# Kernel tuning notes

Hardware: AMD Instinct MI355X
Metric: run time of the kernel (lower is better)

The kernel has to match this reference:

```python
import jax, jax.numpy as jnp
import numpy as np
import math

B, C, H, W = 8, 512, 32, 32
ENC = 1024
L2 = 64
NH = 8
GROUPS = 32
EPS = 1e-5

def group_norm(x, gamma, beta):
    # x: (B, C, L) GroupNorm with 32 groups (float32)
    b, c, l = x.shape
    xg = x.reshape(b, GROUPS, (c // GROUPS) * l)
    mean = xg.mean(-1, keepdims=True)
    var = xg.var(-1, keepdims=True)
    xn = ((xg - mean) * jax.lax.rsqrt(var + EPS)).reshape(b, c, l)
    return xn * gamma[None, :, None] + beta[None, :, None]

def conv1x1(w, bias, x):
    # conv_nd(1, in, out, 1): w (out, in), x (B, in, L) -> (B, out, L)
    return jnp.einsum('oc,bcl->bol', w, x) + bias[None, :, None]

def setup_inputs() -> dict:
    key = jax.random.key(0)
    ks = jax.random.split(key, 16)
    s = lambda fan_in: 1.0 / math.sqrt(fan_in)
    inp = {
        'x': jax.random.normal(ks[0], (B, C, H, W), jnp.float32),
        'xf_out': jax.random.normal(ks[1], (B, ENC, L2), jnp.float32),
        'obj_class_embedding': jax.random.normal(ks[2], (B, ENC, L2), jnp.float32),
        'obj_bbox_embedding': jax.random.normal(ks[3], (B, ENC, L2), jnp.float32),
        'image_patch_bbox_embedding': jax.random.normal(ks[4], (B, ENC, H * W), jnp.float32),
        'key_padding_mask': jax.random.bernoulli(ks[5], 0.3, (B, L2)),
        'qkv_w': jax.random.normal(ks[6], (3 * C, C), jnp.float32) * s(C),
        'qkv_b': jnp.zeros((3 * C,), jnp.float32),
        'g_qkv': jnp.ones((C,), jnp.float32),
        'b_qkv': jnp.zeros((C,), jnp.float32),
        'lc_w': jax.random.normal(ks[7], (2 * C, ENC), jnp.float32) * s(ENC),
        'lc_b': jnp.zeros((2 * C,), jnp.float32),
        'lp_w': jax.random.normal(ks[8], (C, ENC), jnp.float32) * s(ENC),
        'lp_b': jnp.zeros((C,), jnp.float32),
        'g_obj': jnp.ones((ENC,), jnp.float32),
        'b_obj': jnp.zeros((ENC,), jnp.float32),
        'g_lpos': jnp.ones((C,), jnp.float32),
        'b_lpos': jnp.zeros((C,), jnp.float32),
        'g_ipos': jnp.ones((C,), jnp.float32),
        'b_ipos': jnp.zeros((C,), jnp.float32),
        # proj_out is zero-initialized in the original (zero_module); use random
        # weights so the projection math is exercised non-trivially.
        'proj_w': jax.random.normal(ks[9], (C, C), jnp.float32) * s(C),
        'proj_b': jnp.zeros((C,), jnp.float32),
    }
    return inp

def reference(x, xf_out, obj_class_embedding, obj_bbox_embedding,
              image_patch_bbox_embedding, key_padding_mask,
              qkv_w, qkv_b, g_qkv, b_qkv, lc_w, lc_b, lp_w, lp_b,
              g_obj, b_obj, g_lpos, b_lpos, g_ipos, b_ipos, proj_w, proj_b):
    b, c, h, w = x.shape
    L1 = h * w
    d = C // NH
    xf = x.reshape(b, c, L1)

    qkv = conv1x1(qkv_w, qkv_b, group_norm(xf, g_qkv, b_qkv))  # (B, 3C, L1)
    q, k, v = jnp.split(qkv, 3, axis=1)
    q = q.reshape(b * NH, d, L1)
    k = k.reshape(b * NH, d, L1)
    v = v.reshape(b * NH, d, L1)

    ipp = group_norm(conv1x1(lp_w, lp_b, image_patch_bbox_embedding), g_ipos, b_ipos)
    ipp = ipp.reshape(b * NH, d, L1)

    q_img = jnp.concatenate([q, ipp], axis=1)  # (B*H, 2d, L1)
    k_img = jnp.concatenate([k, ipp], axis=1)

    lpe = group_norm(conv1x1(lp_w, lp_b, obj_bbox_embedding), g_lpos, b_lpos)
    lpe = lpe.reshape(b * NH, d, L2)

    lce = (xf_out + group_norm(obj_class_embedding, g_obj, b_obj)) / 2
    kl, vl = jnp.split(conv1x1(lc_w, lc_b, lce), 2, axis=1)
    kl = kl.reshape(b * NH, d, L2)
    vl = vl.reshape(b * NH, d, L2)
    k_layout = jnp.concatenate([kl, lpe], axis=1)  # (B*H, 2d, L2)

    k_mix = jnp.concatenate([k_img, k_layout], axis=2)  # (B*H, 2d, L1+L2)
    v_mix = jnp.concatenate([v, vl], axis=2)             # (B*H, d, L1+L2)

    mask = jnp.concatenate([jnp.zeros((b, L1), bool), key_padding_mask], axis=1)  # (B, L1+L2)

    scale = 1.0 / math.sqrt(math.sqrt(2 * C // NH))
    attn = jnp.einsum('bct,bcs->bts', q_img * scale, k_mix * scale)  # (B*H, L1, L1+L2)
    attn = attn.reshape(b, NH, L1, L1 + L2)
    attn = jnp.where(mask[:, None, None, :], -jnp.inf, attn)
    attn = jax.nn.softmax(attn.astype(jnp.float32), axis=-1).astype(attn.dtype)
    attn = attn.reshape(b * NH, L1, L1 + L2)

    out = jnp.einsum('bts,bcs->bct', attn, v_mix).reshape(b, C, L1)
    hproj = conv1x1(proj_w, proj_b, out)
    return (xf + hproj).reshape(b, c, h, w)
```

## Files before the change

kernel.cpp:

```cpp
#include <hip/hip_runtime.h>
#include <math.h>

#define NB 8
#define NC 512
#define NL1 1024
#define NL2 64
#define NLKV 1088
#define NENC 1024
#define EPSV 1e-5f
#define SCALE2 0.08838834764831845f
#define SCALE2Q 0.12752425f
#define DEFER_THR 11.5415603f

typedef _Float16 half8 __attribute__((ext_vector_type(8)));
typedef _Float16 half4 __attribute__((ext_vector_type(4)));
typedef __fp16 fp16x2 __attribute__((ext_vector_type(2)));
typedef float f32x4 __attribute__((ext_vector_type(4)));
typedef float f32x16 __attribute__((ext_vector_type(16)));

__device__ __forceinline__ void gload16(const _Float16* g, _Float16* l) {
  __builtin_amdgcn_global_load_lds(
      (const __attribute__((address_space(1))) void*)g,
      (__attribute__((address_space(3))) void*)l, 16, 0, 0);
}

__device__ __forceinline__ unsigned int pkrtz(float a, float b) {
  union { fp16x2 hh; unsigned int uu; } cv;
  cv.hh = __builtin_amdgcn_cvt_pkrtz(a, b);
  return cv.uu;
}

__device__ __forceinline__ float fast_exp2(float x) {
  return __builtin_amdgcn_exp2f(x);
}

__global__ __launch_bounds__(256) void k_init(
    const float* __restrict__ x, const float* __restrict__ obj,
    float* __restrict__ xm, float* __restrict__ xr,
    float* __restrict__ om, float* __restrict__ orr,
    const float* __restrict__ qkv_w, _Float16* __restrict__ w16qkv,
    const float* __restrict__ lp_w, _Float16* __restrict__ w16lp,
    const float* __restrict__ proj_w, _Float16* __restrict__ w16proj,
    const float* __restrict__ lc_w, _Float16* __restrict__ w16lc)
{
  int bid = blockIdx.x;
  if (bid < 512) {
    const float* p; float* meanp; float* rstdp; int n, bg;
    if (bid < 256) {
      bg = bid;
      int b = bg >> 5, g = bg & 31;
      p = x + ((size_t)b * 512 + (size_t)g * 16) * 1024;
      n = 16 * 1024; meanp = xm; rstdp = xr;
    } else {
      bg = bid - 256;
      int b = bg >> 5, g = bg & 31;
      p = obj + ((size_t)b * 1024 + (size_t)g * 32) * 64;
      n = 32 * 64; meanp = om; rstdp = orr;
    }
    float s = 0.f, s2 = 0.f;
    for (int i = threadIdx.x; i < n; i += 256) { float v = p[i]; s += v; s2 += v * v; }
    #pragma unroll
    for (int o = 32; o > 0; o >>= 1) { s += __shfl_down(s, o); s2 += __shfl_down(s2, o); }
    __shared__ float rs[4], rq[4];
    int lane = threadIdx.x & 63, w = threadIdx.x >> 6;
    if (lane == 0) { rs[w] = s; rq[w] = s2; }
    __syncthreads();
    if (threadIdx.x == 0) {
      float S = rs[0] + rs[1] + rs[2] + rs[3];
      float Q = rq[0] + rq[1] + rq[2] + rq[3];
      float m = S / n;
      float v = Q / n - m * m;
      if (v < 0.f) v = 0.f;
      meanp[bg] = m;
      rstdp[bg] = rsqrtf(v + EPSV);
    }
  } else {
    int cb = bid - 512;
    const float* s; _Float16* d; int i4;
    if (cb < 768)        { s = qkv_w;  d = w16qkv;  i4 = cb * 256 + threadIdx.x; }
    else if (cb < 1280)  { s = lp_w;   d = w16lp;   i4 = (cb - 768) * 256 + threadIdx.x; }
    else if (cb < 1536)  { s = proj_w; d = w16proj; i4 = (cb - 1280) * 256 + threadIdx.x; }
    else                 { s = lc_w;   d = w16lc;   i4 = (cb - 1536) * 256 + threadIdx.x; }
    float4 v = *(const float4*)&s[(size_t)i4 * 4];
    half4 o; o.x = (_Float16)v.x; o.y = (_Float16)v.y; o.z = (_Float16)v.z; o.w = (_Float16)v.w;
    *(half4*)&d[(size_t)i4 * 4] = o;
  }
}

__global__ __launch_bounds__(256) void k_prep(
    const float* __restrict__ x, const float* __restrict__ xm, const float* __restrict__ xr,
    const float* __restrict__ g_qkv, const float* __restrict__ b_qkv, _Float16* __restrict__ xT,
    const float* __restrict__ ipbe, _Float16* __restrict__ ipbeT,
    const float* __restrict__ xf_out, const float* __restrict__ obj_class,
    const float* __restrict__ obj_bbox,
    const float* __restrict__ om, const float* __restrict__ orr,
    const float* __restrict__ g_obj, const float* __restrict__ b_obj,
    _Float16* __restrict__ lceT, _Float16* __restrict__ objT)
{
  __shared__ _Float16 tile[64][72];
  const int bid = blockIdx.x;
  const int tl = threadIdx.x & 63;
  if (bid < 1024) {
    const int tt = bid & 15, ct = (bid >> 4) & 7, b = bid >> 7;
    const int c0 = ct * 64, t0 = tt * 64;
    const int cp = threadIdx.x >> 6;
    #pragma unroll
    for (int i = 0; i < 16; i++) {
      int c = c0 + i * 4 + cp;
      float v = x[((size_t)b * NC + c) * NL1 + t0 + tl];
      int g = c >> 4;
      float ga = g_qkv[c] * xr[b * 32 + g];
      float be = b_qkv[c] - xm[b * 32 + g] * ga;
      tile[tl][i * 4 + cp] = (_Float16)(v * ga + be);
    }
    __syncthreads();
    int tr = threadIdx.x >> 2, c16 = (threadIdx.x & 3) * 16;
    _Float16* dst = xT + ((size_t)b * 1024 + t0 + tr) * 512 + c0 + c16;
    *(half8*)dst = *(half8*)&tile[tr][c16];
    *(half8*)(dst + 8) = *(half8*)&tile[tr][c16 + 8];
  } else if (bid < 3072) {
    const int e2 = bid - 1024;
    const int tt = e2 & 15, et = (e2 >> 4) & 15, b = e2 >> 8;
    const int e0 = et * 64, t0 = tt * 64;
    const int ep = threadIdx.x >> 6;
    #pragma unroll
    for (int i = 0; i < 16; i++) {
      int e = e0 + i * 4 + ep;
      tile[tl][i * 4 + ep] = (_Float16)ipbe[((size_t)b * 1024 + e) * 1024 + t0 + tl];
    }
    __syncthreads();
    int tr = threadIdx.x >> 2, c16 = (threadIdx.x & 3) * 16;
    _Float16* d = ipbeT + ((size_t)b * 1024 + t0 + tr) * 1024 + e0 + c16;
    *(half8*)d = *(half8*)&tile[tr][c16];
    *(half8*)(d + 8) = *(half8*)&tile[tr][c16 + 8];
  } else {
    const int e2 = bid - 3072;
    const int et = e2 & 15, which = (e2 >> 4) & 1, b = e2 >> 5;
    const int e0 = et * 64;
    const int ep = threadIdx.x >> 6;
    if (which == 0) {
      #pragma unroll
      for (int i = 0; i < 16; i++) {
        int e = e0 + i * 4 + ep;
        size_t idx = ((size_t)b * 1024 + e) * 64 + tl;
        int g = e >> 5;
        float xn = (obj_class[idx] - om[b * 32 + g]) * orr[b * 32 + g] * g_obj[e] + b_obj[e];
        tile[tl][i * 4 + ep] = (_Float16)(0.5f * (xf_out[idx] + xn));
      }
    } else {
      #pragma unroll
      for (int i = 0; i < 16; i++) {
        int e = e0 + i * 4 + ep;
        tile[tl][i * 4 + ep] = (_Float16)obj_bbox[((size_t)b * 1024 + e) * 64 + tl];
      }
    }
    __syncthreads();
    int tr = threadIdx.x >> 2, c16 = (threadIdx.x & 3) * 16;
    _Float16* dst = (which == 0 ? lceT : objT) + ((size_t)b * 64 + tr) * 1024 + e0 + c16;
    *(half8*)dst = *(half8*)&tile[tr][c16];
    *(half8*)(dst + 8) = *(half8*)&tile[tr][c16 + 8];
  }
}

#define MFMA_CORE(KTOT)                                                                  \
  f32x4 acc[4][4];                                                                       \
  _Pragma("unroll") for (int i_ = 0; i_ < 4; i_++)                                       \
      _Pragma("unroll") for (int j_ = 0; j_ < 4; j_++) acc[i_][j_] = (f32x4)0.f;         \
  {                                                                                      \
    const int rsub = lane >> 3, csrc = (lane & 7) ^ rsub;                                \
    for (int kt = 0; kt < (KTOT); kt += 64) {                                            \
      _Pragma("unroll") for (int i = 0; i < 4; i++) {                                    \
        int seg = w * 4 + i;                                                             \
        int row = seg * 8 + rsub;                                                        \
        gload16(Abase + (size_t)(m0 + row) * (KTOT) + kt + csrc * 8, ldsA + seg * 512);  \
        gload16(Bbase + (size_t)(n0 + row) * (KTOT) + kt + csrc * 8, ldsB + seg * 512);  \
      }                                                                                  \
      __syncthreads();                                                                   \
      _Pragma("unroll") for (int kk = 0; kk < 2; kk++) {                                 \
        half8 af[4], bf[4];                                                              \
        _Pragma("unroll") for (int mb = 0; mb < 4; mb++) {                               \
          int row = wm + mb * 16 + l15;                                                  \
          af[mb] = *(const half8*)((const char*)ldsA + row * 128 +                       \
                                   ((kk * 64 + lg * 16) ^ ((row & 7) << 4)));            \
        }                                                                                \
        _Pragma("unroll") for (int nb = 0; nb < 4; nb++) {                               \
          int row = wn + nb * 16 + l15;                                                  \
          bf[nb] = *(const half8*)((const char*)ldsB + row * 128 +                       \
                                   ((kk * 64 + lg * 16) ^ ((row & 7) << 4)));            \
        }                                                                                \
        _Pragma("unroll") for (int mb = 0; mb < 4; mb++)                                 \
            _Pragma("unroll") for (int nb = 0; nb < 4; nb++)                             \
                acc[mb][nb] = __builtin_amdgcn_mfma_f32_16x16x32_f16(af[mb], bf[nb],     \
                                                                    acc[mb][nb], 0, 0, 0);\
      }                                                                                  \
      __syncthreads();                                                                   \
    }                                                                                    \
  }

#define MFMA_CORE_N64(KTOT)                                                              \
  f32x4 acc[4][2];                                                                       \
  _Pragma("unroll") for (int i_ = 0; i_ < 4; i_++)                                       \
      _Pragma("unroll") for (int j_ = 0; j_ < 2; j_++) acc[i_][j_] = (f32x4)0.f;         \
  {                                                                                      \
    const int rsub = lane >> 3, csrc = (lane & 7) ^ rsub;                                \
    for (int kt = 0; kt < (KTOT); kt += 64) {                                            \
      _Pragma("unroll") for (int i = 0; i < 4; i++) {                                    \
        int seg = w * 4 + i;                                                             \
        int row = seg * 8 + rsub;                                                        \
        gload16(Abase + (size_t)(m0 + row) * (KTOT) + kt + csrc * 8, ldsA + seg * 512);  \
      }                                                                                  \
      _Pragma("unroll") for (int i = 0; i < 2; i++) {                                    \
        int seg = w * 2 + i;                                                             \
        int row = seg * 8 + rsub;                                                        \
        gload16(Bbase + (size_t)row * (KTOT) + kt + csrc * 8, ldsB + seg * 512);         \
      }                                                                                  \
      __syncthreads();                                                                   \
      _Pragma("unroll") for (int kk = 0; kk < 2; kk++) {                                 \
        half8 af[4], bf[2];                                                              \
        _Pragma("unroll") for (int mb = 0; mb < 4; mb++) {                               \
          int row = wm + mb * 16 + l15;                                                  \
          af[mb] = *(const half8*)((const char*)ldsA + row * 128 +                       \
                                   ((kk * 64 + lg * 16) ^ ((row & 7) << 4)));            \
        }                                                                                \
        _Pragma("unroll") for (int nb = 0; nb < 2; nb++) {                               \
          int row = wn + nb * 16 + l15;                                                  \
          bf[nb] = *(const half8*)((const char*)ldsB + row * 128 +                       \
                                   ((kk * 64 + lg * 16) ^ ((row & 7) << 4)));            \
        }                                                                                \
        _Pragma("unroll") for (int mb = 0; mb < 4; mb++)                                 \
            _Pragma("unroll") for (int nb = 0; nb < 2; nb++)                             \
                acc[mb][nb] = __builtin_amdgcn_mfma_f32_16x16x32_f16(af[mb], bf[nb],     \
                                                                    acc[mb][nb], 0, 0, 0);\
      }                                                                                  \
      __syncthreads();                                                                   \
    }                                                                                    \
  }

__global__ __launch_bounds__(256) void k_mfma_big(
    const _Float16* __restrict__ w16qkv, const float* __restrict__ qkv_b,
    const _Float16* __restrict__ xhatT,
    const _Float16* __restrict__ w16lp, const float* __restrict__ lp_b,
    const _Float16* __restrict__ ipbeT,
    const _Float16* __restrict__ w16lc, const float* __restrict__ lc_b,
    const _Float16* __restrict__ lceT, const _Float16* __restrict__ objT,
    const float* __restrict__ g_lpos, const float* __restrict__ b_lpos,
    _Float16* __restrict__ qT, _Float16* __restrict__ kT, _Float16* __restrict__ vT,
    _Float16* __restrict__ ipp16)
{
  __shared__ _Float16 smem[16384];
  const int bid = blockIdx.x;
  const int tid = threadIdx.x, lane = tid & 63, w = tid >> 6;
  const int l15 = lane & 15, lg = lane >> 4;

  if (bid < 768) {
    const int nt = bid & 7, tt = bid >> 3;
    const int mt = tt % 12, b = tt / 12;
    const int m0 = mt * 128, n0 = nt * 128;
    _Float16* ldsA = smem;
    _Float16* ldsB = smem + 8192;
    const _Float16* Abase = w16qkv;
    const _Float16* Bbase = xhatT + (size_t)b * 1024 * 512;
    const int wm = (w >> 1) * 64, wn = (w & 1) * 64;
    MFMA_CORE(512)

    char* tb = (char*)smem;
    if (m0 < 1024) {
      const bool isq = (m0 < 512);
      const float qs = isq ? SCALE2Q : 1.f;
      #pragma unroll
      for (int mb = 0; mb < 4; mb++) {
        #pragma unroll
        for (int r = 0; r < 4; r++) {
          int mcol = wm + mb * 16 + lg * 4 + r;
          float bia = qkv_b[m0 + mcol];
          #pragma unroll
          for (int nb = 0; nb < 4; nb++) {
            int trow = wn + nb * 16 + l15;
            float val = (acc[mb][nb][r] + bia) * qs;
            *(_Float16*)(tb + ((trow * 256 + mcol * 2) ^ ((trow & 7) << 4))) = (_Float16)val;
          }
        }
      }
      __syncthreads();
      #pragma unroll
      for (int it = 0; it < 8; it++) {
        int e = it * 256 + tid;
        int trow = e >> 4, seg = e & 15;
        half8 v = *(const half8*)(tb + ((trow * 256 + seg * 16) ^ ((trow & 7) << 4)));
        if (isq) {
          int mq = m0 + seg * 8, hh = mq >> 6, dc = mq & 63;
          *(half8*)(qT + (((size_t)b * 8 + hh) * 1024 + n0 + trow) * 128 + dc) = v;
        } else {
          int mk = m0 - 512 + seg * 8, hh = mk >> 6, dc = mk & 63;
          *(half8*)(kT + (((size_t)b * 8 + hh) * 1088 + n0 + trow) * 128 + dc) = v;
        }
      }
    } else {
      #pragma unroll
      for (int mb = 0; mb < 4; mb++) {
        #pragma unroll
        for (int r = 0; r < 4; r++) {
          int mrow = wm + mb * 16 + lg * 4 + r;
          float bia = qkv_b[m0 + mrow];
          #pragma unroll
          for (int nb = 0; nb < 4; nb++) {
            int tcol = wn + nb * 16 + l15;
            *(_Float16*)(tb + ((mrow * 256 + tcol * 2) ^ ((mrow & 7) << 4))) =
                (_Float16)(acc[mb][nb][r] + bia);
          }
        }
      }
      __syncthreads();
      #pragma unroll
      for (int it = 0; it < 8; it++) {
        int e = it * 256 + tid;
        int mrow = e >> 4, seg = e & 15;
        half8 v = *(const half8*)(tb + ((mrow * 256 + seg * 16) ^ ((mrow & 7) << 4)));
        int mv = m0 - 1024 + mrow, hh = mv >> 6, dc = mv & 63;
        *(half8*)(vT + (((size_t)b * 8 + hh) * 64 + dc) * 1088 + n0 + seg * 8) = v;
      }
    }
  } else if (bid < 1280) {
    const int local = bid - 768;
    const int nt = local & 15, mt = (local >> 4) & 3, b = local >> 6;
    const int m0 = mt * 128, n0 = nt * 64;
    _Float16* ldsA = smem;
    _Float16* ldsB = smem + 8192;
    const _Float16* Abase = w16lp;
    const _Float16* Bbase = ipbeT + (size_t)b * 1024 * 1024 + (size_t)n0 * 1024;
    const int wm = (w >> 1) * 64, wn = (w & 1) * 32;
    MFMA_CORE_N64(1024)
    #pragma unroll
    for (int mb = 0; mb < 4; mb++) {
      #pragma unroll
      for (int r = 0; r < 4; r++) {
        int m = m0 + wm + mb * 16 + lg * 4 + r;
        float bia = lp_b[m];
        #pragma unroll
        for (int nb = 0; nb < 2; nb++) {
          int t = n0 + wn + nb * 16 + l15;
          ipp16[((size_t)b * NC + m) * NL1 + t] = (_Float16)(acc[mb][nb][r] + bia);
        }
      }
    }
  } else {
    const int local = bid - 1280;
    const int mt = local % 12, b = local / 12;
    const bool islc = (mt < 8);
    const int m0 = (islc ? mt : mt - 8) * 128;
    _Float16* ldsA = smem;
    _Float16* ldsB = smem + 8192;
    float (*red_s)[4] = (float(*)[4])(smem + 12288);
    float (*red_q)[4] = (float(*)[4])(smem + 12320);
    const _Float16* Abase = islc ? w16lc : w16lp;
    const float* bias = islc ? lc_b : lp_b;
    const _Float16* Bbase = (islc ? lceT : objT) + (size_t)b * 64 * 1024;
    const int wm = (w >> 1) * 64, wn = (w & 1) * 32;
    MFMA_CORE_N64(1024)

    if (islc) {
      #pragma unroll
      for (int mb = 0; mb < 4; mb++) {
        #pragma unroll
        for (int r = 0; r < 4; r++) {
          int m = m0 + wm + mb * 16 + lg * 4 + r;
          float bia = bias[m];
          #pragma unroll
          for (int nb = 0; nb < 2; nb++) {
            int l = wn + nb * 16 + l15;
            float val = acc[mb][nb][r] + bia;
            if (m < 512) {
              int h = m >> 6, dc = m & 63;
              kT[(((size_t)b * 8 + h) * 1088 + 1024 + l) * 128 + dc] = (_Float16)val;
            } else {
              int mv = m - 512, h = mv >> 6, dc = mv & 63;
              vT[(((size_t)b * 8 + h) * 64 + dc) * 1088 + 1024 + l] = (_Float16)val;
            }
          }
        }
      }
    } else {
      float vals[4][2][4];
      float ps[4], pq[4];
      #pragma unroll
      for (int mb = 0; mb < 4; mb++) {
        ps[mb] = 0.f; pq[mb] = 0.f;
        #pragma unroll
        for (int r = 0; r < 4; r++) {
          int m = m0 + wm + mb * 16 + lg * 4 + r;
          float bia = bias[m];
          #pragma unroll
          for (int nb = 0; nb < 2; nb++) {
            float val = acc[mb][nb][r] + bia;
            vals[mb][nb][r] = val;
            ps[mb] += val; pq[mb] += val * val;
          }
        }
      }
      #pragma unroll
      for (int mb = 0; mb < 4; mb++) {
        #pragma unroll
        for (int o = 32; o > 0; o >>= 1) {
          ps[mb] += __shfl_xor(ps[mb], o);
          pq[mb] += __shfl_xor(pq[mb], o);
        }
      }
      if (lane == 0) {
        #pragma unroll
        for (int mb = 0; mb < 4; mb++) { red_s[w][mb] = ps[mb]; red_q[w][mb] = pq[mb]; }
      }
      __syncthreads();
      const int wbase = (wm >> 6) * 2;
      #pragma unroll
      for (int mb = 0; mb < 4; mb++) {
        float S = red_s[wbase][mb] + red_s[wbase + 1][mb];
        float Q = red_q[wbase][mb] + red_q[wbase + 1][mb];
        float mean = S * (1.f / 1024.f);
        float var = Q * (1.f / 1024.f) - mean * mean;
        if (var < 0.f) var = 0.f;
        float rstd = rsqrtf(var + EPSV);
        #pragma unroll
        for (int r = 0; r < 4; r++) {
          int c = m0 + wm + mb * 16 + lg * 4 + r;
          float ga = g_lpos[c] * rstd;
          float be = b_lpos[c] - mean * ga;
          int hh = c >> 6, dc = c & 63;
          #pragma unroll
          for (int nb = 0; nb < 2; nb++) {
            int l = wn + nb * 16 + l15;
            float xn = vals[mb][nb][r] * ga + be;
            kT[(((size_t)b * 8 + hh) * 1088 + 1024 + l) * 128 + 64 + dc] = (_Float16)xn;
          }
        }
      }
    }
  }
}

__global__ __launch_bounds__(256) void k_mfma_proj(
    const _Float16* __restrict__ Abase, const float* __restrict__ bias,
    const _Float16* __restrict__ Ball, const float* __restrict__ xin,
    float* __restrict__ out)
{
  __shared__ _Float16 ldsA[128 * 64];
  __shared__ _Float16 ldsB[64 * 64];
  const int b = blockIdx.z, mt = blockIdx.y, nt = blockIdx.x;
  const int m0 = mt * 128, n0 = nt * 64;
  const _Float16* Bbase = Ball + (size_t)b * 1024 * 512 + (size_t)n0 * 512;
  const int tid = threadIdx.x, lane = tid & 63, w = tid >> 6;
  const int l15 = lane & 15, lg = lane >> 4;
  const int wm = (w >> 1) * 64, wn = (w & 1) * 32;
  MFMA_CORE_N64(512)
  #pragma unroll
  for (int mb = 0; mb < 4; mb++) {
    #pragma unroll
    for (int r = 0; r < 4; r++) {
      int m = m0 + wm + mb * 16 + lg * 4 + r;
      float bia = bias[m];
      #pragma unroll
      for (int nb = 0; nb < 2; nb++) {
        int t = n0 + wn + nb * 16 + l15;
        size_t idx = ((size_t)b * NC + m) * NL1 + t;
        out[idx] = xin[idx] + acc[mb][nb][r] + bia;
      }
    }
  }
}

__global__ __launch_bounds__(256) void k_ipp_fuse(
    const _Float16* __restrict__ raw,
    const float* __restrict__ gm, const float* __restrict__ gb,
    _Float16* __restrict__ qT, _Float16* __restrict__ kT)
{
  const int g = blockIdx.x, b = blockIdx.y;
  const int tid = threadIdx.x;
  const _Float16* p = raw + ((size_t)b * 512 + (size_t)g * 16) * 1024;
  const int t0 = tid * 4;

  float4 v[16];
  float s = 0.f, s2 = 0.f;
  #pragma unroll
  for (int c = 0; c < 16; c++) {
    half4 hv = *(const half4*)&p[(size_t)c * 1024 + t0];
    v[c].x = (float)hv.x; v[c].y = (float)hv.y; v[c].z = (float)hv.z; v[c].w = (float)hv.w;
    s += v[c].x + v[c].y + v[c].z + v[c].w;
    s2 += v[c].x * v[c].x + v[c].y * v[c].y + v[c].z * v[c].z + v[c].w * v[c].w;
  }
  #pragma unroll
  for (int o = 32; o > 0; o >>= 1) { s += __shfl_down(s, o); s2 += __shfl_down(s2, o); }
  __shared__ float rs[4], rq[4], stat[2];
  int lane = tid & 63, w = tid >> 6;
  if (lane == 0) { rs[w] = s; rq[w] = s2; }
  __syncthreads();
  if (tid == 0) {
    float S = rs[0] + rs[1] + rs[2] + rs[3];
    float Q = rq[0] + rq[1] + rq[2] + rq[3];
    float mn = S / 16384.f;
    float var = Q / 16384.f - mn * mn;
    if (var < 0.f) var = 0.f;
    stat[0] = mn; stat[1] = rsqrtf(var + EPSV);
  }
  __syncthreads();
  const float mn = stat[0], rstd = stat[1];

  float ga[16], be[16];
  #pragma unroll
  for (int c = 0; c < 16; c++) {
    ga[c] = gm[g * 16 + c] * rstd;
    be[c] = gb[g * 16 + c] - mn * ga[c];
  }

  const size_t bh = (size_t)b * 8 + (g >> 2);
  const int dcb = (g & 3) * 16;
  #pragma unroll
  for (int j = 0; j < 4; j++) {
    const int t = t0 + j;
    half8 k0, k1, q0, q1;
    #pragma unroll
    for (int c = 0; c < 8; c++) {
      float4 vc = v[c];
      float e = (j == 0) ? vc.x : (j == 1) ? vc.y : (j == 2) ? vc.z : vc.w;
      float xn = e * ga[c] + be[c];
      k0[c] = (_Float16)xn;
      q0[c] = (_Float16)(SCALE2Q * xn);
    }
    #pragma unroll
    for (int c = 8; c < 16; c++) {
      float4 vc = v[c];
      float e = (j == 0) ? vc.x : (j == 1) ? vc.y : (j == 2) ? vc.z : vc.w;
      float xn = e * ga[c] + be[c];
      k1[c - 8] = (_Float16)xn;
      q1[c - 8] = (_Float16)(SCALE2Q * xn);
    }
    _Float16* qd = qT + (bh * 1024 + t) * 128 + 64 + dcb;
    _Float16* kd = kT + (bh * 1088 + t) * 128 + 64 + dcb;
    *(half8*)qd = q0; *(half8*)(qd + 8) = q1;
    *(half8*)kd = k0; *(half8*)(kd + 8) = k1;
  }
}

__global__ __launch_bounds__(256) void k_attn_mfma(
    const _Float16* __restrict__ qT, const _Float16* __restrict__ kT,
    const _Float16* __restrict__ vT, const int* __restrict__ mask,
    _Float16* __restrict__ attnT)
{
  const int x = blockIdx.x & 7;
  const int k = blockIdx.x >> 3;
  const int bh = x + ((k >> 3) << 3);
  const int qt = k & 7;
  const int b = bh >> 3, h = bh & 7;
  const int tid = threadIdx.x;
  const int lane = tid & 63;
  const int w = tid >> 6;
  const int l31 = lane & 31;
  const int hi = lane >> 5;

  __shared__ _Float16 KsB[2 * 64 * 128];
  __shared__ _Float16 VtB[2 * 64 * 64];

  const int q = qt * 128 + w * 32 + l31;

  half8 aq[8];
  {
    const _Float16* qp = qT + ((size_t)bh * 1024 + q) * 128 + hi * 8;
    #pragma unroll
    for (int kst = 0; kst < 8; kst++) aq[kst] = *(const half8*)(qp + kst * 16);
  }

  unsigned int mbits = 0;
  {
    const int* mp = mask + b * 64;
    #pragma unroll
    for (int sb = 0; sb < 2; sb++) {
      #pragma unroll
      for (int reg = 0; reg < 16; reg++) {
        int s = sb * 32 + (reg & 3) + 8 * (reg >> 2) + 4 * hi;
        if (mp[s]) mbits |= 1u << (sb * 16 + reg);
      }
    }
  }

  f32x16 O0 = (f32x16)0.f, O1 = (f32x16)0.f;
  float m_run = -INFINITY, l_run = 0.f;

  const int kxor = (l31 & 7) << 4;
  const int ksrow_off = lane >> 4;
  const int kcsrc_base = lane & 15;
  const int vdc_off = lane >> 3;
  const int vcsrc_base = lane & 7;

#define STAGE_KV(T, KD, VD)                                                          \
  {                                                                                  \
    const int s0_ = (T) * 64;                                                        \
    _Pragma("unroll") for (int r = 0; r < 4; r++) {                                  \
      int seg = r * 4 + w;                                                           \
      int srow = seg * 4 + ksrow_off;                                                \
      int csrc = kcsrc_base ^ (srow & 7);                                            \
      gload16(kT + ((size_t)bh * 1088 + s0_ + srow) * 128 + csrc * 8, (KD) + seg * 512); \
    }                                                                                \
    _Pragma("unroll") for (int r = 0; r < 2; r++) {                                  \
      int seg = r * 4 + w;                                                           \
      int dc = seg * 8 + vdc_off;                                                    \
      int csrc = vcsrc_base ^ (dc & 7);                                              \
      gload16(vT + ((size_t)bh * 64 + dc) * 1088 + s0_ + csrc * 8, (VD) + seg * 512);  \
    }                                                                                \
  }

  STAGE_KV(0, KsB, VtB)
  asm volatile("s_waitcnt vmcnt(0)" ::: "memory");
  __builtin_amdgcn_s_barrier();

  int cur = 0;
  for (int t = 0; t < 17; t++) {
    if (t < 16) {
      _Float16* kd = KsB + ((cur ^ 1) << 13);
      _Float16* vd = VtB + ((cur ^ 1) << 12);
      STAGE_KV(t + 1, kd, vd)
    }
    const char* ksb = (const char*)(KsB + (cur << 13));
    const char* vtb = (const char*)(VtB + (cur << 12));

    f32x16 sc0 = (f32x16)0.f, sc1 = (f32x16)0.f;
    __builtin_amdgcn_s_setprio(1);
    #pragma unroll
    for (int kst = 0; kst < 8; kst++) {
      half8 kf0 = *(const half8*)(ksb + ((l31 * 256 + kst * 32 + hi * 16) ^ kxor));
      half8 kf1 = *(const half8*)(ksb + (((32 + l31) * 256 + kst * 32 + hi * 16) ^ kxor));
      sc0 = __builtin_amdgcn_mfma_f32_32x32x16_f16(kf0, aq[kst], sc0, 0, 0, 0);
      sc1 = __builtin_amdgcn_mfma_f32_32x32x16_f16(kf1, aq[kst], sc1, 0, 0, 0);
    }
    __builtin_amdgcn_s_setprio(0);

    if (t == 16) {
      #pragma unroll
      for (int i = 0; i < 16; i++) {
        if ((mbits >> i) & 1)        sc0[i] = -INFINITY;
        if ((mbits >> (16 + i)) & 1) sc1[i] = -INFINITY;
      }
    }

    float mx;
    {
      float a0 = fmaxf(fmaxf(sc0[0], sc0[1]), sc0[2]);
      float a1 = fmaxf(fmaxf(sc0[3], sc0[4]), sc0[5]);
      float a2 = fmaxf(fmaxf(sc0[6], sc0[7]), sc0[8]);
      float a3 = fmaxf(fmaxf(sc0[9], sc0[10]), sc0[11]);
      float a4 = fmaxf(fmaxf(sc0[12], sc0[13]), sc0[14]);
      float a5 = fmaxf(fmaxf(sc0[15], sc1[0]), sc1[1]);
      float a6 = fmaxf(fmaxf(sc1[2], sc1[3]), sc1[4]);
      float a7 = fmaxf(fmaxf(sc1[5], sc1[6]), sc1[7]);
      float a8 = fmaxf(fmaxf(sc1[8], sc1[9]), sc1[10]);
      float a9 = fmaxf(fmaxf(sc1[11], sc1[12]), sc1[13]);
      float aa = fmaxf(sc1[14], sc1[15]);
      float b0 = fmaxf(fmaxf(a0, a1), a2);
      float b1 = fmaxf(fmaxf(a3, a4), a5);
      float b2 = fmaxf(fmaxf(a6, a7), a8);
      float b3 = fmaxf(a9, aa);
      mx = fmaxf(fmaxf(b0, b1), fmaxf(b2, b3));
    }
    mx = fmaxf(mx, __shfl_xor(mx, 32));
    if (__all(mx <= m_run + DEFER_THR)) {
      float sum = 0.f;
      #pragma unroll
      for (int i = 0; i < 16; i++) { float p = fast_exp2(sc0[i] - m_run); sc0[i] = p; sum += p; }
      #pragma unroll
      for (int i = 0; i < 16; i++) { float p = fast_exp2(sc1[i] - m_run); sc1[i] = p; sum += p; }
      sum += __shfl_xor(sum, 32);
      l_run += sum;
    } else {
      float m_new = fmaxf(m_run, mx);
      float alpha = fast_exp2(m_run - m_new);
      float sum = 0.f;
      #pragma unroll
      for (int i = 0; i < 16; i++) { float p = fast_exp2(sc0[i] - m_new); sc0[i] = p; sum += p; }
      #pragma unroll
      for (int i = 0; i < 16; i++) { float p = fast_exp2(sc1[i] - m_new); sc1[i] = p; sum += p; }
      sum += __shfl_xor(sum, 32);
      l_run = l_run * alpha + sum;
      m_run = m_new;
      #pragma unroll
      for (int i = 0; i < 16; i++) { O0[i] *= alpha; O1[i] *= alpha; }
    }

    __builtin_amdgcn_s_setprio(1);
    #pragma unroll
    for (int sb = 0; sb < 2; sb++) {
      #pragma unroll
      for (int k2 = 0; k2 < 2; k2++) {
        const int kst = sb * 2 + k2;
        unsigned int pa0, pa1, pb0, pb1;
        if (sb == 0) {
          pa0 = pkrtz(sc0[8 * k2 + 0], sc0[8 * k2 + 1]);
          pa1 = pkrtz(sc0[8 * k2 + 2], sc0[8 * k2 + 3]);
          pb0 = pkrtz(sc0[8 * k2 + 4], sc0[8 * k2 + 5]);
          pb1 = pkrtz(sc0[8 * k2 + 6], sc0[8 * k2 + 7]);
        } else {
          pa0 = pkrtz(sc1[8 * k2 + 0], sc1[8 * k2 + 1]);
          pa1 = pkrtz(sc1[8 * k2 + 2], sc1[8 * k2 + 3]);
          pb0 = pkrtz(sc1[8 * k2 + 4], sc1[8 * k2 + 5]);
          pb1 = pkrtz(sc1[8 * k2 + 6], sc1[8 * k2 + 7]);
        }
        unsigned int keep0 = hi ? pb0 : pa0, keep1 = hi ? pb1 : pa1;
        unsigned int send0 = hi ? pa0 : pb0, send1 = hi ? pa1 : pb1;
        unsigned int recv0 = (unsigned int)__shfl_xor((int)send0, 32);
        unsigned int recv1 = (unsigned int)__shfl_xor((int)send1, 32);
        union { unsigned int u[4]; half8 hh; } pf;
        pf.u[0] = hi ? recv0 : keep0;
        pf.u[1] = hi ? recv1 : keep1;
        pf.u[2] = hi ? keep0 : recv0;
        pf.u[3] = hi ? keep1 : recv1;

        half8 vf0 = *(const half8*)(vtb + ((l31 * 128 + kst * 32 + hi * 16) ^ kxor));
        half8 vf1 = *(const half8*)(vtb + (((32 + l31) * 128 + kst * 32 + hi * 16) ^ kxor));
        O0 = __builtin_amdgcn_mfma_f32_32x32x16_f16(vf0, pf.hh, O0, 0, 0, 0);
        O1 = __builtin_amdgcn_mfma_f32_32x32x16_f16(vf1, pf.hh, O1, 0, 0, 0);
      }
    }
    __builtin_amdgcn_s_setprio(0);

    asm volatile("s_waitcnt vmcnt(0)" ::: "memory");
    __builtin_amdgcn_s_barrier();
    cur ^= 1;
  }

  float inv = 1.f / l_run;
  _Float16* op = attnT + ((size_t)b * 1024 + q) * 512 + h * 64;
  #pragma unroll
  for (int i = 0; i < 16; i += 2) {
    int dc = (i & 3) + 8 * (i >> 2) + 4 * hi;
    unsigned int c0 = pkrtz(O0[i] * inv, O0[i + 1] * inv);
    unsigned int c1 = pkrtz(O1[i] * inv, O1[i + 1] * inv);
    *(unsigned int*)(op + dc) = c0;
    *(unsigned int*)(op + 32 + dc) = c1;
  }
}

extern "C" void kernel_launch(void* const* d_in, const int* in_sizes, int n_in,
                              void* d_out, int out_size, void* d_ws, size_t ws_size,
                              hipStream_t stream) {
  const float* x         = (const float*)d_in[0];
  const float* xf_out    = (const float*)d_in[1];
  const float* obj_class = (const float*)d_in[2];
  const float* obj_bbox  = (const float*)d_in[3];
  const float* ipbe      = (const float*)d_in[4];
  const int*   mask      = (const int*)d_in[5];
  const float* qkv_w     = (const float*)d_in[6];
  const float* qkv_b     = (const float*)d_in[7];
  const float* g_qkv     = (const float*)d_in[8];
  const float* b_qkv     = (const float*)d_in[9];
  const float* lc_w      = (const float*)d_in[10];
  const float* lc_b      = (const float*)d_in[11];
  const float* lp_w      = (const float*)d_in[12];
  const float* lp_b      = (const float*)d_in[13];
  const float* g_obj     = (const float*)d_in[14];
  const float* b_obj     = (const float*)d_in[15];
  const float* g_lpos    = (const float*)d_in[16];
  const float* b_lpos    = (const float*)d_in[17];
  const float* g_ipos    = (const float*)d_in[18];
  const float* b_ipos    = (const float*)d_in[19];
  const float* proj_w    = (const float*)d_in[20];
  const float* proj_b    = (const float*)d_in[21];
  float* out = (float*)d_out;

  _Float16* f16b = (_Float16*)d_ws;
  _Float16* qT      = f16b;
  _Float16* kT      = qT + 8388608;
  _Float16* vT      = kT + 8912896;
  _Float16* xhatT   = vT + 4456448;
  _Float16* ipbeT   = xhatT + 4194304;
  _Float16* attnT   = ipbeT + 8388608;
  _Float16* w16qkv  = attnT + 4194304;
  _Float16* w16lp   = w16qkv + 786432;
  _Float16* w16proj = w16lp + 524288;
  _Float16* w16lc   = w16proj + 262144;
  _Float16* lceT    = w16lc + 1048576;
  _Float16* objT    = lceT + 524288;
  _Float16* ipp16   = objT + 524288;
  float* st = (float*)(ipp16 + 4194304);
  float* xm = st, * xr = st + 256, * om = st + 512, * orr = st + 768;

  dim3 blk(256);
  k_init<<<dim3(3072), blk, 0, stream>>>(x, obj_class, xm, xr, om, orr,
                                         qkv_w, w16qkv, lp_w, w16lp, proj_w, w16proj, lc_w, w16lc);
  k_prep<<<dim3(3328), blk, 0, stream>>>(x, xm, xr, g_qkv, b_qkv, xhatT,
                                         ipbe, ipbeT,
                                         xf_out, obj_class, obj_bbox, om, orr, g_obj, b_obj,
                                         lceT, objT);
  k_mfma_big<<<dim3(1376), blk, 0, stream>>>(w16qkv, qkv_b, xhatT,
                                             w16lp, lp_b, ipbeT,
                                             w16lc, lc_b, lceT, objT,
                                             g_lpos, b_lpos,
                                             qT, kT, vT, ipp16);
  k_ipp_fuse<<<dim3(32, 8), blk, 0, stream>>>(ipp16, g_ipos, b_ipos, qT, kT);
  k_attn_mfma<<<dim3(512), blk, 0, stream>>>(qT, kT, vT, mask, attnT);
  k_mfma_proj<<<dim3(16, 4, 8), blk, 0, stream>>>(w16proj, proj_b, attnT, x, out);
}
```

Before: 147.7 us.

## Double-buffer LDS tiles in MFMA GEMM cores and reorder block dispatch

Converts both MFMA GEMM core macros to a double-buffered LDS scheme, so the next K-tile's global-to-LDS loads are issued before the current tile's MFMAs and each iteration drops one barrier. Shared memory per block doubles, which can lower occupancy. The fused projection kernel also remaps block IDs so the long K=1024 layout and position GEMM blocks are scheduled ahead of the QKV blocks, aiming to shorten the tail.

```diff
diff --git a/kernel.cpp b/kernel.cpp
--- a/kernel.cpp
+++ b/kernel.cpp
@@ -168,24 +168,39 @@
       _Pragma("unroll") for (int j_ = 0; j_ < 4; j_++) acc[i_][j_] = (f32x4)0.f;         \
   {                                                                                      \
     const int rsub = lane >> 3, csrc = (lane & 7) ^ rsub;                                \
-    for (int kt = 0; kt < (KTOT); kt += 64) {                                            \
-      _Pragma("unroll") for (int i = 0; i < 4; i++) {                                    \
-        int seg = w * 4 + i;                                                             \
-        int row = seg * 8 + rsub;                                                        \
-        gload16(Abase + (size_t)(m0 + row) * (KTOT) + kt + csrc * 8, ldsA + seg * 512);  \
-        gload16(Bbase + (size_t)(n0 + row) * (KTOT) + kt + csrc * 8, ldsB + seg * 512);  \
+    const int NT_ = (KTOT) / 64;                                                         \
+    _Pragma("unroll") for (int i = 0; i < 4; i++) {                                      \
+      int seg = w * 4 + i;                                                               \
+      int row = seg * 8 + rsub;                                                          \
+      gload16(Abase + (size_t)(m0 + row) * (KTOT) + csrc * 8, ldsA + seg * 512);         \
+      gload16(Bbase + (size_t)(n0 + row) * (KTOT) + csrc * 8, ldsB + seg * 512);         \
+    }                                                                                    \
+    __syncthreads();                                                                     \
+    int cur_ = 0;                                                                        \
+    for (int t_ = 0; t_ < NT_; t_++) {                                                   \
+      if (t_ + 1 < NT_) {                                                                \
+        _Float16* da_ = ldsA + ((cur_ ^ 1) << 13);                                       \
+        _Float16* db_ = ldsB + ((cur_ ^ 1) << 13);                                       \
+        int kt = (t_ + 1) * 64;                                                          \
+        _Pragma("unroll") for (int i = 0; i < 4; i++) {                                  \
+          int seg = w * 4 + i;                                                           \
+          int row = seg * 8 + rsub;                                                      \
+          gload16(Abase + (size_t)(m0 + row) * (KTOT) + kt + csrc * 8, da_ + seg * 512); \
+          gload16(Bbase + (size_t)(n0 + row) * (KTOT) + kt + csrc * 8, db_ + seg * 512); \
+        }                                                                                \
       }                                                                                  \
-      __syncthreads();                                                                   \
+      const char* ra_ = (const char*)(ldsA + (cur_ << 13));                              \
+      const char* rb_ = (const char*)(ldsB + (cur_ << 13));                              \
       _Pragma("unroll") for (int kk = 0; kk < 2; kk++) {                                 \
         half8 af[4], bf[4];                                                              \
         _Pragma("unroll") for (int mb = 0; mb < 4; mb++) {                               \
           int row = wm + mb * 16 + l15;                                                  \
-          af[mb] = *(const half8*)((const char*)ldsA + row * 128 +                       \
+          af[mb] = *(const half8*)(ra_ + row * 128 +                                     \
                                    ((kk * 64 + lg * 16) ^ ((row & 7) << 4)));            \
         }                                                                                \
         _Pragma("unroll") for (int nb = 0; nb < 4; nb++) {                               \
           int row = wn + nb * 16 + l15;                                                  \
-          bf[nb] = *(const half8*)((const char*)ldsB + row * 128 +                       \
+          bf[nb] = *(const half8*)(rb_ + row * 128 +                                     \
                                    ((kk * 64 + lg * 16) ^ ((row & 7) << 4)));            \
         }                                                                                \
         _Pragma("unroll") for (int mb = 0; mb < 4; mb++)                                 \
@@ -194,6 +209,7 @@
                                                                     acc[mb][nb], 0, 0, 0);\
       }                                                                                  \
       __syncthreads();                                                                   \
+      cur_ ^= 1;                                                                         \
     }                                                                                    \
   }
 
@@ -203,28 +219,47 @@
       _Pragma("unroll") for (int j_ = 0; j_ < 2; j_++) acc[i_][j_] = (f32x4)0.f;         \
   {                                                                                      \
     const int rsub = lane >> 3, csrc = (lane & 7) ^ rsub;                                \
-    for (int kt = 0; kt < (KTOT); kt += 64) {                                            \
-      _Pragma("unroll") for (int i = 0; i < 4; i++) {                                    \
-        int seg = w * 4 + i;                                                             \
-        int row = seg * 8 + rsub;                                                        \
-        gload16(Abase + (size_t)(m0 + row) * (KTOT) + kt + csrc * 8, ldsA + seg * 512);  \
+    const int NT_ = (KTOT) / 64;                                                         \
+    _Pragma("unroll") for (int i = 0; i < 4; i++) {                                      \
+      int seg = w * 4 + i;                                                               \
+      int row = seg * 8 + rsub;                                                          \
+      gload16(Abase + (size_t)(m0 + row) * (KTOT) + csrc * 8, ldsA + seg * 512);         \
+    }                                                                                    \
+    _Pragma("unroll") for (int i = 0; i < 2; i++) {                                      \
+      int seg = w * 2 + i;                                                               \
+      int row = seg * 8 + rsub;                                                          \
+      gload16(Bbase + (size_t)row * (KTOT) + csrc * 8, ldsB + seg * 512);                \
+    }                                                                                    \
+    __syncthreads();                                                                     \
+    int cur_ = 0;                                                                        \
+    for (int t_ = 0; t_ < NT_; t_++) {                                                   \
+      if (t_ + 1 < NT_) {                                                                \
+        _Float16* da_ = ldsA + ((cur_ ^ 1) << 13);                                       \
+        _Float16* db_ = ldsB + ((cur_ ^ 1) << 12);                                       \
+        int kt = (t_ + 1) * 64;                                                          \
+        _Pragma("unroll") for (int i = 0; i < 4; i++) {                                  \
+          int seg = w * 4 + i;                                                           \
+          int row = seg * 8 + rsub;                                                      \
+          gload16(Abase + (size_t)(m0 + row) * (KTOT) + kt + csrc * 8, da_ + seg * 512); \
+        }                                                                                \
+        _Pragma("unroll") for (int i = 0; i < 2; i++) {                                  \
+          int seg = w * 2 + i;                                                           \
+          int row = seg * 8 + rsub;                                                      \
+          gload16(Bbase + (size_t)row * (KTOT) + kt + csrc * 8, db_ + seg * 512);        \
+        }                                                                                \
       }                                                                                  \
-      _Pragma("unroll") for (int i = 0; i < 2; i++) {                                    \
-        int seg = w * 2 + i;                                                             \
-        int row = seg * 8 + rsub;                                                        \
-        gload16(Bbase + (size_t)row * (KTOT) + kt + csrc * 8, ldsB + seg * 512);         \
-      }                                                                                  \
-      __syncthreads();                                                                   \
+      const char* ra_ = (const char*)(ldsA + (cur_ << 13));                              \
+      const char* rb_ = (const char*)(ldsB + (cur_ << 12));                              \
       _Pragma("unroll") for (int kk = 0; kk < 2; kk++) {                                 \
         half8 af[4], bf[2];                                                              \
         _Pragma("unroll") for (int mb = 0; mb < 4; mb++) {                               \
           int row = wm + mb * 16 + l15;                                                  \
-          af[mb] = *(const half8*)((const char*)ldsA + row * 128 +                       \
+          af[mb] = *(const half8*)(ra_ + row * 128 +                                     \
                                    ((kk * 64 + lg * 16) ^ ((row & 7) << 4)));            \
         }                                                                                \
         _Pragma("unroll") for (int nb = 0; nb < 2; nb++) {                               \
           int row = wn + nb * 16 + l15;                                                  \
-          bf[nb] = *(const half8*)((const char*)ldsB + row * 128 +                       \
+          bf[nb] = *(const half8*)(rb_ + row * 128 +                                     \
                                    ((kk * 64 + lg * 16) ^ ((row & 7) << 4)));            \
         }                                                                                \
         _Pragma("unroll") for (int mb = 0; mb < 4; mb++)                                 \
@@ -233,6 +268,7 @@
                                                                     acc[mb][nb], 0, 0, 0);\
       }                                                                                  \
       __syncthreads();                                                                   \
+      cur_ ^= 1;                                                                         \
     }                                                                                    \
   }
 
@@ -247,8 +283,9 @@
     _Float16* __restrict__ qT, _Float16* __restrict__ kT, _Float16* __restrict__ vT,
     _Float16* __restrict__ ipp16)
 {
-  __shared__ _Float16 smem[16384];
-  const int bid = blockIdx.x;
+  __shared__ _Float16 smem[32768];
+  const int bid0 = blockIdx.x;
+  const int bid = (bid0 < 608) ? (bid0 + 768) : (bid0 - 608);
   const int tid = threadIdx.x, lane = tid & 63, w = tid >> 6;
   const int l15 = lane & 15, lg = lane >> 4;
 
@@ -257,7 +294,7 @@
     const int mt = tt % 12, b = tt / 12;
     const int m0 = mt * 128, n0 = nt * 128;
     _Float16* ldsA = smem;
-    _Float16* ldsB = smem + 8192;
+    _Float16* ldsB = smem + 16384;
     const _Float16* Abase = w16qkv;
     const _Float16* Bbase = xhatT + (size_t)b * 1024 * 512;
     const int wm = (w >> 1) * 64, wn = (w & 1) * 64;
@@ -325,7 +362,7 @@
     const int nt = local & 15, mt = (local >> 4) & 3, b = local >> 6;
     const int m0 = mt * 128, n0 = nt * 64;
     _Float16* ldsA = smem;
-    _Float16* ldsB = smem + 8192;
+    _Float16* ldsB = smem + 16384;
     const _Float16* Abase = w16lp;
     const _Float16* Bbase = ipbeT + (size_t)b * 1024 * 1024 + (size_t)n0 * 1024;
     const int wm = (w >> 1) * 64, wn = (w & 1) * 32;
@@ -349,9 +386,9 @@
     const bool islc = (mt < 8);
     const int m0 = (islc ? mt : mt - 8) * 128;
     _Float16* ldsA = smem;
-    _Float16* ldsB = smem + 8192;
-    float (*red_s)[4] = (float(*)[4])(smem + 12288);
-    float (*red_q)[4] = (float(*)[4])(smem + 12320);
+    _Float16* ldsB = smem + 16384;
+    float (*red_s)[4] = (float(*)[4])(smem + 24576);
+    float (*red_q)[4] = (float(*)[4])(smem + 24608);
     const _Float16* Abase = islc ? w16lc : w16lp;
     const float* bias = islc ? lc_b : lp_b;
     const _Float16* Bbase = (islc ? lceT : objT) + (size_t)b * 64 * 1024;
@@ -442,8 +479,9 @@
     const _Float16* __restrict__ Ball, const float* __restrict__ xin,
     float* __restrict__ out)
 {
-  __shared__ _Float16 ldsA[128 * 64];
-  __shared__ _Float16 ldsB[64 * 64];
+  __shared__ _Float16 smem[24576];
+  _Float16* ldsA = smem;
+  _Float16* ldsB = smem + 16384;
   const int b = blockIdx.z, mt = blockIdx.y, nt = blockIdx.x;
   const int m0 = mt * 128, n0 = nt * 64;
   const _Float16* Bbase = Ball + (size_t)b * 1024 * 512 + (size_t)n0 * 512;
```

New measurement: 138.2 us. 1.07x faster.
